# Optimization experiments

Measured on AMD Instinct MI355X. Metric: run time of the kernel, lower is better.

## Reference

```python
import jax, jax.numpy as jnp
import numpy as np

B, T, D, H, E, TOP_K = 2, 2048, 1024, 4096, 8, 2


def setup_inputs() -> dict:
    key = jax.random.key(0)
    ks = jax.random.split(key, 7)
    s_d = 1.0 / np.sqrt(D)
    s_h = 1.0 / np.sqrt(H)
    return {
        "x": jax.random.normal(ks[0], (B, T, D), dtype=jnp.float32),
        "gate_w": jax.random.uniform(ks[1], (D, E), minval=-s_d, maxval=s_d, dtype=jnp.float32),
        "gate_b": jax.random.uniform(ks[2], (E,), minval=-s_d, maxval=s_d, dtype=jnp.float32),
        "w1": jax.random.uniform(ks[3], (E, D, H), minval=-s_d, maxval=s_d, dtype=jnp.float32),
        "b1": jax.random.uniform(ks[4], (E, H), minval=-s_d, maxval=s_d, dtype=jnp.float32),
        "w2": jax.random.uniform(ks[5], (E, H, D), minval=-s_h, maxval=s_h, dtype=jnp.float32),
        "b2": jax.random.uniform(ks[6], (E, D), minval=-s_h, maxval=s_h, dtype=jnp.float32),
    }


def reference(x, gate_w, gate_b, w1, b1, w2, b2):
    Bsz, Tn, Din = x.shape
    x_flat = x.reshape(-1, Din)                       # [N, D]
    N = x_flat.shape[0]
    gating_logits = x_flat @ gate_w + gate_b          # [N, E]
    weights, indices = jax.lax.top_k(gating_logits, TOP_K)
    weights = jax.nn.softmax(weights, axis=-1).astype(x.dtype)
    # scatter top-k weights into dense dispatch tensor [N, E]
    dispatch = jnp.zeros((N, E), dtype=x.dtype).at[jnp.arange(N)[:, None], indices].set(weights)
    # NOTE: faithful to original - gate weight multiplies the expert INPUT
    # and again the expert OUTPUT (double weighting through the GELU MLP).
    dispatched_x = dispatch[:, :, None] * x_flat[:, None, :]       # [N, E, D]
    h = jax.nn.gelu(jnp.einsum('ned,edh->neh', dispatched_x, w1) + b1, approximate=False)
    expert_out = jnp.einsum('neh,ehd->ned', h, w2) + b2            # [N, E, D]
    combined = jnp.sum(dispatch[:, :, None] * expert_out, axis=1)  # [N, D]
    final = combined.reshape(Bsz, Tn, -1)
    return final, gating_logits
```

## Files before the change

### kernel.cpp

```cpp
#include <hip/hip_runtime.h>
#include <hip/hip_bf16.h>
#include <math.h>

#define NTOK 4096
#define DDIM 1024
#define HDIM 4096
#define NEXP 8
#define CAP  4096
#define ROWCAP 10240
#define MAXTILES 40

typedef __attribute__((ext_vector_type(8))) short short8;
typedef __attribute__((ext_vector_type(4))) float f32x4;

#define GLOAD_LDS16(g, l) __builtin_amdgcn_global_load_lds( \
    (const __attribute__((address_space(1))) void*)(g),     \
    (__attribute__((address_space(3))) void*)(l), 16, 0, 0)

__global__ __launch_bounds__(256) void gating_kernel(
    const float* __restrict__ x, const float* __restrict__ gw,
    const float* __restrict__ gb, float* __restrict__ logits_out,
    int* __restrict__ counts, int* __restrict__ tok, float* __restrict__ gate,
    int* __restrict__ eA, int* __restrict__ sA, float* __restrict__ gA) {
  int t = blockIdx.x;
  int tid = threadIdx.x;
  float p[NEXP];
#pragma unroll
  for (int e = 0; e < NEXP; ++e) p[e] = 0.f;
  const float* xr = x + (size_t)t * DDIM;
  for (int d = tid; d < DDIM; d += 256) {
    float xv = xr[d];
    const float* wr = gw + (size_t)d * NEXP;
#pragma unroll
    for (int e = 0; e < NEXP; ++e) p[e] += xv * wr[e];
  }
#pragma unroll
  for (int off = 32; off > 0; off >>= 1)
#pragma unroll
    for (int e = 0; e < NEXP; ++e) p[e] += __shfl_xor(p[e], off, 64);
  __shared__ float red[4][NEXP];
  int wave = tid >> 6, lane = tid & 63;
  if (lane == 0)
#pragma unroll
    for (int e = 0; e < NEXP; ++e) red[wave][e] = p[e];
  __syncthreads();
  if (tid < NEXP) {
    float v = red[0][tid] + red[1][tid] + red[2][tid] + red[3][tid] + gb[tid];
    logits_out[(size_t)t * NEXP + tid] = v;
    red[0][tid] = v;
  }
  __syncthreads();
  if (tid == 0) {
    float v[NEXP];
#pragma unroll
    for (int e = 0; e < NEXP; ++e) v[e] = red[0][e];
    int i0 = 0;
#pragma unroll
    for (int e = 1; e < NEXP; ++e) if (v[e] > v[i0]) i0 = e;
    int i1 = (i0 == 0) ? 1 : 0;
#pragma unroll
    for (int e = 0; e < NEXP; ++e) if (e != i0 && v[e] > v[i1]) i1 = e;
    float e1 = expf(v[i1] - v[i0]);
    float s = 1.f + e1;
    float g0 = 1.f / s, g1 = e1 / s;
    int s0 = atomicAdd(&counts[i0], 1);
    tok[i0 * CAP + s0] = t; gate[i0 * CAP + s0] = g0;
    int s1 = atomicAdd(&counts[i1], 1);
    tok[i1 * CAP + s1] = t; gate[i1 * CAP + s1] = g1;
    eA[2 * t] = i0; sA[2 * t] = s0; gA[2 * t] = g0;
    eA[2 * t + 1] = i1; sA[2 * t + 1] = s1; gA[2 * t + 1] = g1;
  }
}

__global__ void sched_kernel(const int* __restrict__ counts, int* __restrict__ poff,
                             int* __restrict__ tileE, int* __restrict__ tileR,
                             int* __restrict__ nTiles) {
  if (threadIdx.x == 0) {
    int acc = 0, nt = 0;
    for (int e = 0; e < NEXP; ++e) {
      poff[e] = acc;
      int tl = (counts[e] + 255) >> 8;
      for (int t = 0; t < tl; ++t) { tileE[nt] = e; tileR[nt] = acc + t * 256; ++nt; }
      acc += tl << 8;
    }
    poff[NEXP] = acc;
    nTiles[0] = nt;
  }
}

__global__ __launch_bounds__(256) void transpose_all(
    const float* __restrict__ w1, const float* __restrict__ w2,
    __hip_bfloat16* __restrict__ wT1, __hip_bfloat16* __restrict__ wT2) {
  __shared__ float tile[64 * 65];
  int id = blockIdx.x;
  const float* inp; __hip_bfloat16* outp; int R, C, bx, by;
  if (id < 8192) {
    int e = id >> 10, rem = id & 1023;
    bx = rem & 63; by = rem >> 6;
    R = 1024; C = 4096;
    inp = w1 + (size_t)e * R * C; outp = wT1 + (size_t)e * R * C;
  } else {
    id -= 8192;
    int e = id >> 10, rem = id & 1023;
    bx = rem & 15; by = rem >> 4;
    R = 4096; C = 1024;
    inp = w2 + (size_t)e * R * C; outp = wT2 + (size_t)e * R * C;
  }
  int c0 = bx * 64, r0 = by * 64;
  int tx = threadIdx.x & 15, ty = threadIdx.x >> 4;
#pragma unroll
  for (int i = 0; i < 64; i += 16) {
    float4 v = *(const float4*)(inp + (size_t)(r0 + ty + i) * C + c0 + tx * 4);
    float* dst = tile + (ty + i) * 65 + tx * 4;
    dst[0] = v.x; dst[1] = v.y; dst[2] = v.z; dst[3] = v.w;
  }
  __syncthreads();
  int c = threadIdx.x >> 3;
  int rb = (threadIdx.x & 7) * 8;
#pragma unroll
  for (int p = 0; p < 2; ++p) {
    int cc = c + p * 32;
    union { unsigned short u[8]; short8 v8; } pk;
#pragma unroll
    for (int j = 0; j < 8; ++j) {
      __hip_bfloat16 h = __float2bfloat16(tile[(rb + j) * 65 + cc]);
      pk.u[j] = *(unsigned short*)&h;
    }
    *(short8*)(outp + (size_t)(c0 + cc) * R + r0 + rb) = pk.v8;
  }
}

__global__ __launch_bounds__(256) void gather_kernel(
    const float* __restrict__ x, const int* __restrict__ counts,
    const int* __restrict__ poff, const int* __restrict__ tok,
    const float* __restrict__ gate, __hip_bfloat16* __restrict__ Xg) {
  int e = blockIdx.y, r = blockIdx.x;
  int pc = poff[e + 1] - poff[e];
  if (r >= pc) return;
  int row = poff[e] + r;
  int tid = threadIdx.x;
  __hip_bfloat16* orow = Xg + (size_t)row * DDIM;
  if (r < counts[e]) {
    int t = tok[e * CAP + r];
    float g = gate[e * CAP + r];
    float4 v = ((const float4*)(x + (size_t)t * DDIM))[tid];
    union { unsigned short u[4]; uint2 q; } pk;
    __hip_bfloat16 h0 = __float2bfloat16(v.x * g);
    __hip_bfloat16 h1 = __float2bfloat16(v.y * g);
    __hip_bfloat16 h2 = __float2bfloat16(v.z * g);
    __hip_bfloat16 h3 = __float2bfloat16(v.w * g);
    pk.u[0] = *(unsigned short*)&h0; pk.u[1] = *(unsigned short*)&h1;
    pk.u[2] = *(unsigned short*)&h2; pk.u[3] = *(unsigned short*)&h3;
    ((uint2*)orow)[tid] = pk.q;
  } else {
    uint2 z; z.x = 0; z.y = 0;
    ((uint2*)orow)[tid] = z;
  }
}

template <int EPI>
__global__ __launch_bounds__(512, 2) void moe_gemm(
    const __hip_bfloat16* __restrict__ A, const __hip_bfloat16* __restrict__ B,
    const float* __restrict__ bias, __hip_bfloat16* __restrict__ Hout,
    float* __restrict__ Pout, const int* __restrict__ tileE,
    const int* __restrict__ tileR, const int* __restrict__ nTiles,
    int K, int Nn) {
  int f = blockIdx.y * gridDim.x + blockIdx.x;
  int xcd = f & 7, seq = f >> 3;
  int ct, ty, kz;
  if (EPI == 0) {
    ct = xcd * 2 + (seq & 1); ty = seq >> 1; kz = 0;
  } else {
    ct = xcd & 3; kz = xcd >> 2; ty = seq;
  }
  if (ty >= nTiles[0]) return;
  int e = tileE[ty];
  int rowBase = tileR[ty];
  int colBase = ct * 256;

  __shared__ __align__(16) char LA[65536];
  __shared__ __align__(16) char LB[65536];

  const char* Ae = (const char*)A + (size_t)rowBase * K * 2;
  const char* Be = (const char*)B + ((size_t)e * Nn + colBase) * (size_t)K * 2;

  int tid = threadIdx.x;
  int lane = tid & 63, wave = tid >> 6;
  int wm = (wave >> 2) * 128, wn = (wave & 3) * 64;
  int frm = lane & 15, g = lane >> 4;

  int sr = tid >> 3;
  int sch = (tid & 7) ^ (sr & 7);
  const char* aS = Ae + (size_t)sr * K * 2 + sch * 16;
  const char* bS = Be + (size_t)sr * K * 2 + sch * 16;
  size_t rstep = (size_t)64 * K * 2;

  int f7 = frm & 7;
  int sl0 = (g ^ f7) << 4;
  int sl1 = ((4 + g) ^ f7) << 4;
  const char* rA = LA + (wm + frm) * 128;
  const char* rB = LB + (wn + frm) * 128;

  f32x4 acc[8][4] = {};
  int kPer = (EPI == 1) ? (K >> 1) : K;
  int kLo = kz * kPer;
  int NT = kPer >> 6;
  const char* aP = aS + (size_t)kLo * 2;
  const char* bP = bS + (size_t)kLo * 2;

  auto stageA = [&](int t, int s, int b) {
    GLOAD_LDS16(aP + (size_t)t * 128 + (size_t)s * rstep,
                LA + b * 32768 + s * 8192 + tid * 16);
  };
  auto stageB = [&](int t, int s, int b) {
    GLOAD_LDS16(bP + (size_t)t * 128 + (size_t)s * rstep,
                LB + b * 32768 + s * 8192 + tid * 16);
  };

  stageB(0, 0, 0); stageB(0, 1, 0); stageB(0, 2, 0); stageB(0, 3, 0);
  stageA(0, 0, 0); stageA(0, 2, 0); stageA(0, 1, 0); stageA(0, 3, 0);
  asm volatile("s_waitcnt vmcnt(2)" ::: "memory");
  __builtin_amdgcn_sched_barrier(0);
  __builtin_amdgcn_s_barrier();

  for (int t = 0; t < NT; ++t) {
    int rb = t & 1, sb = rb ^ 1;
    const char* Ab = rA + rb * 32768;
    const char* Bb = rB + rb * 32768;
    bool pre = (t + 1 < NT);
    short8 bfr[4][2];
#pragma unroll 4
    for (int p = 0; p < 4; ++p) {
      short8 af[2][2];
      if (p == 0) {
#pragma unroll
        for (int n = 0; n < 4; ++n) {
          bfr[n][0] = *(const short8*)(Bb + (n * 16) * 128 + sl0);
          bfr[n][1] = *(const short8*)(Bb + (n * 16) * 128 + sl1);
        }
      }
#pragma unroll
      for (int i = 0; i < 2; ++i) {
        af[i][0] = *(const short8*)(Ab + ((p * 2 + i) * 16) * 128 + sl0);
        af[i][1] = *(const short8*)(Ab + ((p * 2 + i) * 16) * 128 + sl1);
      }
      if (pre) {
        if (p == 0)      { stageB(t + 1, 0, sb); stageB(t + 1, 1, sb); }
        else if (p == 1) { stageB(t + 1, 2, sb); stageB(t + 1, 3, sb); }
        else if (p == 2) { stageA(t + 1, 0, sb); stageA(t + 1, 2, sb); }
        else             { stageA(t + 1, 1, sb); stageA(t + 1, 3, sb); }
      }
      __builtin_amdgcn_s_barrier();
      asm volatile("s_waitcnt lgkmcnt(0)" ::: "memory");
      __builtin_amdgcn_sched_barrier(0);
      __builtin_amdgcn_s_setprio(1);
#pragma unroll
      for (int ks = 0; ks < 2; ++ks)
#pragma unroll
        for (int i = 0; i < 2; ++i)
#pragma unroll
          for (int n = 0; n < 4; ++n)
            acc[p * 2 + i][n] = __builtin_amdgcn_mfma_f32_16x16x32_bf16(
                af[i][ks], bfr[n][ks], acc[p * 2 + i][n], 0, 0, 0);
      __builtin_amdgcn_s_setprio(0);
      if (p == 1) {
        if (pre) asm volatile("s_waitcnt vmcnt(4)" ::: "memory");
        else     asm volatile("s_waitcnt vmcnt(0)" ::: "memory");
        __builtin_amdgcn_sched_barrier(0);
      } else if (p == 3 && pre) {
        asm volatile("s_waitcnt vmcnt(2)" ::: "memory");
        __builtin_amdgcn_sched_barrier(0);
      }
      __builtin_amdgcn_s_barrier();
    }
  }

  int cq = lane >> 4, cn = lane & 15;
  if (EPI == 0) {
#pragma unroll
    for (int n = 0; n < 4; ++n) {
      int col = colBase + wn + n * 16 + cn;
      float bv = bias[e * Nn + col];
#pragma unroll
      for (int m = 0; m < 8; ++m) {
#pragma unroll
        for (int r = 0; r < 4; ++r) {
          int row = rowBase + wm + m * 16 + cq * 4 + r;
          float v = acc[m][n][r] + bv;
          float z = 1.5957691f * v * (1.0f + 0.044715f * v * v);
          v = v / (1.0f + __expf(-z));
          Hout[(size_t)row * Nn + col] = __float2bfloat16(v);
        }
      }
    }
  } else {
    float* Pp = Pout + ((size_t)kz * ROWCAP + rowBase) * DDIM;
#pragma unroll
    for (int n = 0; n < 4; ++n) {
      int col = colBase + wn + n * 16 + cn;
#pragma unroll
      for (int m = 0; m < 8; ++m) {
#pragma unroll
        for (int r = 0; r < 4; ++r) {
          int row = wm + m * 16 + cq * 4 + r;
          Pp[(size_t)row * DDIM + col] = acc[m][n][r];
        }
      }
    }
  }
}

__global__ __launch_bounds__(256) void combine_kernel(
    const float* __restrict__ P, const float* __restrict__ b2,
    const int* __restrict__ poff, const int* __restrict__ eA,
    const int* __restrict__ sA, const float* __restrict__ gA,
    float* __restrict__ outF) {
  int t = blockIdx.x, c = threadIdx.x;
  int e0 = eA[2 * t], e1 = eA[2 * t + 1];
  int r0 = poff[e0] + sA[2 * t], r1 = poff[e1] + sA[2 * t + 1];
  float g0 = gA[2 * t], g1 = gA[2 * t + 1];
  float4 a0 = ((const float4*)(P + (size_t)r0 * DDIM))[c];
  float4 a1 = ((const float4*)(P + ((size_t)ROWCAP + r0) * DDIM))[c];
  float4 b0 = ((const float4*)(P + (size_t)r1 * DDIM))[c];
  float4 b1 = ((const float4*)(P + ((size_t)ROWCAP + r1) * DDIM))[c];
  float4 bb0 = ((const float4*)(b2 + (size_t)e0 * DDIM))[c];
  float4 bb1 = ((const float4*)(b2 + (size_t)e1 * DDIM))[c];
  float4 o;
  o.x = g0 * (a0.x + a1.x + bb0.x) + g1 * (b0.x + b1.x + bb1.x);
  o.y = g0 * (a0.y + a1.y + bb0.y) + g1 * (b0.y + b1.y + bb1.y);
  o.z = g0 * (a0.z + a1.z + bb0.z) + g1 * (b0.z + b1.z + bb1.z);
  o.w = g0 * (a0.w + a1.w + bb0.w) + g1 * (b0.w + b1.w + bb1.w);
  ((float4*)(outF + (size_t)t * DDIM))[c] = o;
}

extern "C" void kernel_launch(void* const* d_in, const int* in_sizes, int n_in,
                              void* d_out, int out_size, void* d_ws, size_t ws_size,
                              hipStream_t stream) {
  const float* x  = (const float*)d_in[0];
  const float* gw = (const float*)d_in[1];
  const float* gb = (const float*)d_in[2];
  const float* w1 = (const float*)d_in[3];
  const float* b1 = (const float*)d_in[4];
  const float* w2 = (const float*)d_in[5];
  const float* b2 = (const float*)d_in[6];

  float* outF = (float*)d_out;
  float* outL = outF + (size_t)NTOK * DDIM;

  size_t off = 0;
  char* base = (char*)d_ws;
  auto alloc = [&](size_t bytes) {
    void* r = base + off;
    off += (bytes + 255) & ~(size_t)255;
    return r;
  };
  __hip_bfloat16* wT1 = (__hip_bfloat16*)alloc((size_t)NEXP * HDIM * DDIM * 2);
  __hip_bfloat16* Xg  = (__hip_bfloat16*)alloc((size_t)ROWCAP * DDIM * 2);
  __hip_bfloat16* wT2 = (__hip_bfloat16*)alloc((size_t)NEXP * DDIM * HDIM * 2);
  __hip_bfloat16* Hact= (__hip_bfloat16*)alloc((size_t)ROWCAP * HDIM * 2);
  int*   tok    = (int*)alloc((size_t)NEXP * CAP * 4);
  float* gate   = (float*)alloc((size_t)NEXP * CAP * 4);
  int*   eA     = (int*)alloc((size_t)NTOK * 2 * 4);
  int*   sA     = (int*)alloc((size_t)NTOK * 2 * 4);
  float* gA     = (float*)alloc((size_t)NTOK * 2 * 4);
  int*   counts = (int*)alloc(64);
  int*   poff   = (int*)alloc(64);
  int*   tileE  = (int*)alloc(MAXTILES * 4);
  int*   tileR  = (int*)alloc(MAXTILES * 4);
  int*   nTiles = (int*)alloc(64);
  float* P      = (float*)wT1;

  hipMemsetAsync(counts, 0, 64, stream);
  gating_kernel<<<NTOK, 256, 0, stream>>>(x, gw, gb, outL, counts, tok, gate, eA, sA, gA);
  sched_kernel<<<1, 64, 0, stream>>>(counts, poff, tileE, tileR, nTiles);
  transpose_all<<<16384, 256, 0, stream>>>(w1, w2, wT1, wT2);
  gather_kernel<<<dim3(CAP, NEXP), 256, 0, stream>>>(x, counts, poff, tok, gate, Xg);
  moe_gemm<0><<<dim3(16, MAXTILES * 2 / 2, 1), 512, 0, stream>>>(
      Xg, wT1, b1, Hact, nullptr, tileE, tileR, nTiles, DDIM, HDIM);
  moe_gemm<1><<<dim3(8, MAXTILES, 1), 512, 0, stream>>>(
      Hact, wT2, b2, nullptr, P, tileE, tileR, nTiles, HDIM, DDIM);
  combine_kernel<<<NTOK, 256, 0, stream>>>(P, b2, poff, eA, sA, gA, outF);
}
```

Baseline: 696.7 us.

## Stage GEMM epilogues through LDS, drop sched kernel, restructure transpose and gather

The GEMM epilogues now write results into shared memory and then emit wide coalesced row stores, for both the bf16 GELU output and the fp32 partial sums, replacing scattered 2/4-byte column stores. The separate single-thread scheduling kernel is removed, and each consumer recomputes tile and offset mapping from the expert counts. The weight transpose writes transposed data into LDS and reads float4 rows back. The gather launch becomes a compact 1D grid. Costs are an extra LDS round trip with barriers in each epilogue and redundant per-block prefix computations.

```diff
diff --git a/kernel.cpp b/kernel.cpp
--- a/kernel.cpp
+++ b/kernel.cpp
@@ -16,6 +16,18 @@
 #define GLOAD_LDS16(g, l) __builtin_amdgcn_global_load_lds( \
     (const __attribute__((address_space(1))) void*)(g),     \
     (__attribute__((address_space(3))) void*)(l), 16, 0, 0)
+
+__device__ __forceinline__ int tile_lookup(const int* __restrict__ counts,
+                                           int ty, int& e, int& rowBase) {
+  int acc = 0;
+#pragma unroll
+  for (int ee = 0; ee < NEXP; ++ee) {
+    int tl = (counts[ee] + 255) >> 8;
+    if (ty < tl) { e = ee; rowBase = acc + ty * 256; return 1; }
+    ty -= tl; acc += tl << 8;
+  }
+  return 0;
+}
 
 __global__ __launch_bounds__(256) void gating_kernel(
     const float* __restrict__ x, const float* __restrict__ gw,
@@ -72,26 +84,10 @@
   }
 }
 
-__global__ void sched_kernel(const int* __restrict__ counts, int* __restrict__ poff,
-                             int* __restrict__ tileE, int* __restrict__ tileR,
-                             int* __restrict__ nTiles) {
-  if (threadIdx.x == 0) {
-    int acc = 0, nt = 0;
-    for (int e = 0; e < NEXP; ++e) {
-      poff[e] = acc;
-      int tl = (counts[e] + 255) >> 8;
-      for (int t = 0; t < tl; ++t) { tileE[nt] = e; tileR[nt] = acc + t * 256; ++nt; }
-      acc += tl << 8;
-    }
-    poff[NEXP] = acc;
-    nTiles[0] = nt;
-  }
-}
-
 __global__ __launch_bounds__(256) void transpose_all(
     const float* __restrict__ w1, const float* __restrict__ w2,
     __hip_bfloat16* __restrict__ wT1, __hip_bfloat16* __restrict__ wT2) {
-  __shared__ float tile[64 * 65];
+  __shared__ float tileT[64 * 68];
   int id = blockIdx.x;
   const float* inp; __hip_bfloat16* outp; int R, C, bx, by;
   if (id < 8192) {
@@ -110,39 +106,48 @@
   int tx = threadIdx.x & 15, ty = threadIdx.x >> 4;
 #pragma unroll
   for (int i = 0; i < 64; i += 16) {
-    float4 v = *(const float4*)(inp + (size_t)(r0 + ty + i) * C + c0 + tx * 4);
-    float* dst = tile + (ty + i) * 65 + tx * 4;
-    dst[0] = v.x; dst[1] = v.y; dst[2] = v.z; dst[3] = v.w;
+    int rr = ty + i;
+    float4 v = *(const float4*)(inp + (size_t)(r0 + rr) * C + c0 + tx * 4);
+    tileT[(tx * 4 + 0) * 68 + rr] = v.x;
+    tileT[(tx * 4 + 1) * 68 + rr] = v.y;
+    tileT[(tx * 4 + 2) * 68 + rr] = v.z;
+    tileT[(tx * 4 + 3) * 68 + rr] = v.w;
   }
   __syncthreads();
-  int c = threadIdx.x >> 3;
-  int rb = (threadIdx.x & 7) * 8;
-#pragma unroll
-  for (int p = 0; p < 2; ++p) {
-    int cc = c + p * 32;
-    union { unsigned short u[8]; short8 v8; } pk;
-#pragma unroll
-    for (int j = 0; j < 8; ++j) {
-      __hip_bfloat16 h = __float2bfloat16(tile[(rb + j) * 65 + cc]);
-      pk.u[j] = *(unsigned short*)&h;
-    }
-    *(short8*)(outp + (size_t)(c0 + cc) * R + r0 + rb) = pk.v8;
+  int rb = (threadIdx.x & 15) * 4;
+#pragma unroll
+  for (int p = 0; p < 4; ++p) {
+    int cc = (threadIdx.x >> 4) + p * 16;
+    float4 w = *(const float4*)(&tileT[cc * 68 + rb]);
+    union { unsigned short u[4]; uint2 q; } pk;
+    __hip_bfloat16 h0 = __float2bfloat16(w.x);
+    __hip_bfloat16 h1 = __float2bfloat16(w.y);
+    __hip_bfloat16 h2 = __float2bfloat16(w.z);
+    __hip_bfloat16 h3 = __float2bfloat16(w.w);
+    pk.u[0] = *(unsigned short*)&h0; pk.u[1] = *(unsigned short*)&h1;
+    pk.u[2] = *(unsigned short*)&h2; pk.u[3] = *(unsigned short*)&h3;
+    *(uint2*)(outp + (size_t)(c0 + cc) * R + r0 + rb) = pk.q;
   }
 }
 
 __global__ __launch_bounds__(256) void gather_kernel(
     const float* __restrict__ x, const int* __restrict__ counts,
-    const int* __restrict__ poff, const int* __restrict__ tok,
-    const float* __restrict__ gate, __hip_bfloat16* __restrict__ Xg) {
-  int e = blockIdx.y, r = blockIdx.x;
-  int pc = poff[e + 1] - poff[e];
-  if (r >= pc) return;
-  int row = poff[e] + r;
+    const int* __restrict__ tok, const float* __restrict__ gate,
+    __hip_bfloat16* __restrict__ Xg) {
+  int r = blockIdx.x;
+  int acc = 0, e = -1, idx = 0;
+#pragma unroll
+  for (int ee = 0; ee < NEXP; ++ee) {
+    int sz = (((counts[ee] + 255) >> 8) << 8);
+    if (e < 0 && r < acc + sz) { e = ee; idx = r - acc; }
+    acc += sz;
+  }
+  if (e < 0) return;
   int tid = threadIdx.x;
-  __hip_bfloat16* orow = Xg + (size_t)row * DDIM;
-  if (r < counts[e]) {
-    int t = tok[e * CAP + r];
-    float g = gate[e * CAP + r];
+  __hip_bfloat16* orow = Xg + (size_t)r * DDIM;
+  if (idx < counts[e]) {
+    int t = tok[e * CAP + idx];
+    float g = gate[e * CAP + idx];
     float4 v = ((const float4*)(x + (size_t)t * DDIM))[tid];
     union { unsigned short u[4]; uint2 q; } pk;
     __hip_bfloat16 h0 = __float2bfloat16(v.x * g);
@@ -162,8 +167,7 @@
 __global__ __launch_bounds__(512, 2) void moe_gemm(
     const __hip_bfloat16* __restrict__ A, const __hip_bfloat16* __restrict__ B,
     const float* __restrict__ bias, __hip_bfloat16* __restrict__ Hout,
-    float* __restrict__ Pout, const int* __restrict__ tileE,
-    const int* __restrict__ tileR, const int* __restrict__ nTiles,
+    float* __restrict__ Pout, const int* __restrict__ counts,
     int K, int Nn) {
   int f = blockIdx.y * gridDim.x + blockIdx.x;
   int xcd = f & 7, seq = f >> 3;
@@ -173,13 +177,13 @@
   } else {
     ct = xcd & 3; kz = xcd >> 2; ty = seq;
   }
-  if (ty >= nTiles[0]) return;
-  int e = tileE[ty];
-  int rowBase = tileR[ty];
+  int e, rowBase;
+  if (!tile_lookup(counts, ty, e, rowBase)) return;
   int colBase = ct * 256;
 
-  __shared__ __align__(16) char LA[65536];
-  __shared__ __align__(16) char LB[65536];
+  __shared__ __align__(16) char SMEM[135168];
+  char* LA = SMEM;
+  char* LB = SMEM + 65536;
 
   const char* Ae = (const char*)A + (size_t)rowBase * K * 2;
   const char* Be = (const char*)B + ((size_t)e * Nn + colBase) * (size_t)K * 2;
@@ -279,44 +283,72 @@
   if (EPI == 0) {
 #pragma unroll
     for (int n = 0; n < 4; ++n) {
-      int col = colBase + wn + n * 16 + cn;
-      float bv = bias[e * Nn + col];
+      int col = wn + n * 16 + cn;
+      float bv = bias[e * Nn + colBase + col];
 #pragma unroll
       for (int m = 0; m < 8; ++m) {
 #pragma unroll
         for (int r = 0; r < 4; ++r) {
-          int row = rowBase + wm + m * 16 + cq * 4 + r;
+          int row = wm + m * 16 + cq * 4 + r;
           float v = acc[m][n][r] + bv;
           float z = 1.5957691f * v * (1.0f + 0.044715f * v * v);
           v = v / (1.0f + __expf(-z));
-          Hout[(size_t)row * Nn + col] = __float2bfloat16(v);
+          int w = (col >> 1) ^ (((row >> 2) & 3) << 3);
+          *(__hip_bfloat16*)(SMEM + row * 512 + (w << 2) + ((col & 1) << 1)) =
+              __float2bfloat16(v);
         }
       }
+    }
+    __syncthreads();
+#pragma unroll
+    for (int it = 0; it < 16; ++it) {
+      int row = it * 16 + (tid >> 5), ck = tid & 31;
+      int w = (ck << 2) ^ (((row >> 2) & 3) << 3);
+      short8 v = *(const short8*)(SMEM + row * 512 + (w << 2));
+      *(short8*)(Hout + (size_t)(rowBase + row) * Nn + colBase + ck * 8) = v;
     }
   } else {
     float* Pp = Pout + ((size_t)kz * ROWCAP + rowBase) * DDIM;
-#pragma unroll
-    for (int n = 0; n < 4; ++n) {
-      int col = colBase + wn + n * 16 + cn;
-#pragma unroll
-      for (int m = 0; m < 8; ++m) {
-#pragma unroll
-        for (int r = 0; r < 4; ++r) {
-          int row = wm + m * 16 + cq * 4 + r;
-          Pp[(size_t)row * DDIM + col] = acc[m][n][r];
+    int hhalf = wm >> 7;
+#pragma unroll
+    for (int h = 0; h < 2; ++h) {
+      if (hhalf == h) {
+#pragma unroll
+        for (int n = 0; n < 4; ++n) {
+          int col = wn + n * 16 + cn;
+#pragma unroll
+          for (int m = 0; m < 8; ++m) {
+#pragma unroll
+            for (int r = 0; r < 4; ++r) {
+              int rl = m * 16 + cq * 4 + r;
+              *(float*)(SMEM + rl * 1040 + col * 4) = acc[m][n][r];
+            }
+          }
         }
       }
+      __syncthreads();
+#pragma unroll
+      for (int it = 0; it < 16; ++it) {
+        int rr = it * 8 + (tid >> 6), ck = tid & 63;
+        f32x4 v = *(const f32x4*)(SMEM + rr * 1040 + ck * 16);
+        *(f32x4*)(Pp + (size_t)(h * 128 + rr) * DDIM + colBase + ck * 4) = v;
+      }
+      __syncthreads();
     }
   }
 }
 
 __global__ __launch_bounds__(256) void combine_kernel(
     const float* __restrict__ P, const float* __restrict__ b2,
-    const int* __restrict__ poff, const int* __restrict__ eA,
+    const int* __restrict__ counts, const int* __restrict__ eA,
     const int* __restrict__ sA, const float* __restrict__ gA,
     float* __restrict__ outF) {
   int t = blockIdx.x, c = threadIdx.x;
   int e0 = eA[2 * t], e1 = eA[2 * t + 1];
+  int poff[NEXP + 1]; poff[0] = 0;
+#pragma unroll
+  for (int ee = 0; ee < NEXP; ++ee)
+    poff[ee + 1] = poff[ee] + (((counts[ee] + 255) >> 8) << 8);
   int r0 = poff[e0] + sA[2 * t], r1 = poff[e1] + sA[2 * t + 1];
   float g0 = gA[2 * t], g1 = gA[2 * t + 1];
   float4 a0 = ((const float4*)(P + (size_t)r0 * DDIM))[c];
@@ -364,20 +396,15 @@
   int*   sA     = (int*)alloc((size_t)NTOK * 2 * 4);
   float* gA     = (float*)alloc((size_t)NTOK * 2 * 4);
   int*   counts = (int*)alloc(64);
-  int*   poff   = (int*)alloc(64);
-  int*   tileE  = (int*)alloc(MAXTILES * 4);
-  int*   tileR  = (int*)alloc(MAXTILES * 4);
-  int*   nTiles = (int*)alloc(64);
   float* P      = (float*)wT1;
 
   hipMemsetAsync(counts, 0, 64, stream);
   gating_kernel<<<NTOK, 256, 0, stream>>>(x, gw, gb, outL, counts, tok, gate, eA, sA, gA);
-  sched_kernel<<<1, 64, 0, stream>>>(counts, poff, tileE, tileR, nTiles);
   transpose_all<<<16384, 256, 0, stream>>>(w1, w2, wT1, wT2);
-  gather_kernel<<<dim3(CAP, NEXP), 256, 0, stream>>>(x, counts, poff, tok, gate, Xg);
-  moe_gemm<0><<<dim3(16, MAXTILES * 2 / 2, 1), 512, 0, stream>>>(
-      Xg, wT1, b1, Hact, nullptr, tileE, tileR, nTiles, DDIM, HDIM);
+  gather_kernel<<<ROWCAP, 256, 0, stream>>>(x, counts, tok, gate, Xg);
+  moe_gemm<0><<<dim3(16, MAXTILES, 1), 512, 0, stream>>>(
+      Xg, wT1, b1, Hact, nullptr, counts, DDIM, HDIM);
   moe_gemm<1><<<dim3(8, MAXTILES, 1), 512, 0, stream>>>(
-      Hact, wT2, b2, nullptr, P, tileE, tileR, nTiles, HDIM, DDIM);
-  combine_kernel<<<NTOK, 256, 0, stream>>>(P, b2, poff, eA, sA, gA, outF);
-}
+      Hact, wT2, b2, nullptr, P, counts, HDIM, DDIM);
+  combine_kernel<<<NTOK, 256, 0, stream>>>(P, b2, counts, eA, sA, gA, outF);
+}
```

New measurement: 673.6 us. 1.03x faster.
